# Optimization experiments

Measured on AMD Instinct MI355X. Metric: run time of the kernel, lower is better.

## Reference

```python
import jax, jax.numpy as jnp
import numpy as np

D_MODEL = 1024
D_STATE = 16
D_CONV = 4
EXPAND = 1
D_INNER = EXPAND * D_MODEL  # must equal D_MODEL for original dt_proj shapes to work
BATCH = 2
SEQ = 2048


def silu(x):
    return x * jax.nn.sigmoid(x)


def setup_inputs() -> dict:
    key = jax.random.key(0)
    ks = jax.random.split(key, 8)
    s = 0.02
    return {
        "x": jax.random.normal(ks[0], (BATCH, SEQ, D_MODEL), dtype=jnp.float32),
        "W_in": jax.random.normal(ks[1], (2 * D_INNER, D_MODEL), dtype=jnp.float32) * s,
        "conv_w": jax.random.normal(ks[2], (D_INNER, D_CONV), dtype=jnp.float32) * s,
        "conv_b": jnp.zeros((D_INNER,), dtype=jnp.float32),
        "W_dt": jax.random.normal(ks[3], (D_INNER, D_INNER), dtype=jnp.float32) * s,
        "b_dt": jnp.zeros((D_INNER,), dtype=jnp.float32),
        "A_log": jnp.zeros((D_INNER, D_STATE), dtype=jnp.float32),  # torch: log(ones)=0
        "Bp": jax.random.normal(ks[4], (D_INNER, D_STATE), dtype=jnp.float32),
        "Cp": jax.random.normal(ks[5], (D_INNER, D_STATE), dtype=jnp.float32),
        "Dp": jnp.ones((D_INNER,), dtype=jnp.float32),
        "W_out": jax.random.normal(ks[6], (D_MODEL, D_INNER), dtype=jnp.float32) * s,
    }


def reference(x, W_in, conv_w, conv_b, W_dt, b_dt, A_log, Bp, Cp, Dp, W_out):
    B, L, _ = x.shape
    # in_proj then split into ssm branch and gating residual
    xr = x @ W_in.T                               # (B, L, 2*D_INNER)
    x_proj, res = jnp.split(xr, 2, axis=-1)       # each (B, L, D_INNER)

    # causal depthwise conv1d (kernel D_CONV), == torch conv1d(padding=K-1)[..., :L]
    xp = jnp.pad(x_proj, ((0, 0), (D_CONV - 1, 0), (0, 0)))
    xc = conv_b + sum(conv_w[:, k] * xp[:, k:k + L, :] for k in range(D_CONV))
    xc = silu(xc)                                 # (B, L, D_INNER)

    # selective SSM scan
    delta = jax.nn.softplus(xc @ W_dt.T + b_dt)   # (B, L, D_INNER)
    A = -jnp.exp(A_log)                           # (D_INNER, D_STATE)
    dA = jnp.exp(delta[..., None] * A)            # (B, L, D_INNER, D_STATE)
    dBx = delta[..., None] * Bp * xc[..., None]   # (B, L, D_INNER, D_STATE)

    def step(h, inp):
        dA_t, dBx_t = inp                         # (B, D_INNER, D_STATE)
        h = dA_t * h + dBx_t
        y = jnp.einsum('bdn,dn->bd', h, Cp)
        return h, y

    h0 = jnp.zeros((B, D_INNER, D_STATE), dtype=x.dtype)
    _, ys = jax.lax.scan(step, h0, (dA.transpose(1, 0, 2, 3), dBx.transpose(1, 0, 2, 3)))
    x_ssm = ys.transpose(1, 0, 2) + xc * Dp       # (B, L, D_INNER)

    return (x_ssm * silu(res)) @ W_out.T          # (B, L, D_MODEL)
```

## Files before the change

### kernel.cpp

```cpp
#include <hip/hip_runtime.h>

typedef unsigned short u16;
typedef __bf16 bf16;
typedef bf16 bf16x8 __attribute__((ext_vector_type(8)));
typedef float f32x4 __attribute__((ext_vector_type(4)));

#define SEQ     2048
#define BATCH   2
#define DM      1024
#define DI      1024
#define NROW    (BATCH*SEQ)
#define NSTATE  16
#define NCHUNK  64
#define CLEN    32
#define BK      64

static_assert(SEQ == NCHUNK * CLEN, "chunking must cover SEQ");

__device__ __forceinline__ u16 f2bf(float f) {
  unsigned u = __builtin_bit_cast(unsigned, f);
  u += 0x7FFFu + ((u >> 16) & 1u);
  return (u16)(u >> 16);
}
__device__ __forceinline__ float bf2f(u16 u) {
  return __builtin_bit_cast(float, (unsigned)u << 16);
}
__device__ __forceinline__ float sigm(float x) { return 1.f / (1.f + __expf(-x)); }

__global__ __launch_bounds__(256) void k_cvt_all(
    const float* __restrict__ x, const float* __restrict__ Win,
    const float* __restrict__ Wdt, const float* __restrict__ Wout,
    u16* __restrict__ xbf, u16* __restrict__ winbf,
    u16* __restrict__ wdtbf, u16* __restrict__ woutbf)
{
  long i = (long)blockIdx.x * 256 + threadIdx.x;
  const float* src; u16* dst; long off;
  if (i < 1048576)            { src = x;    dst = xbf;    off = i; }
  else if (i < 1572864)       { src = Win;  dst = winbf;  off = i - 1048576; }
  else if (i < 1835008)       { src = Wdt;  dst = wdtbf;  off = i - 1572864; }
  else                        { src = Wout; dst = woutbf; off = i - 1835008; }
  float4 v = reinterpret_cast<const float4*>(src)[off];
  ushort4 o;
  o.x = f2bf(v.x); o.y = f2bf(v.y); o.z = f2bf(v.z); o.w = f2bf(v.w);
  reinterpret_cast<ushort4*>(dst)[off] = o;
}


__device__ __forceinline__ void gload16(const u16* g, u16* l) {
  __builtin_amdgcn_global_load_lds((const __attribute__((address_space(1))) void*)g,
                                   (__attribute__((address_space(3))) void*)l,
                                   16, 0, 0);
}

template<int EPI, int BM, int BN, int GX>
__global__ __launch_bounds__(256, 4) void k_gemm(
    const u16* __restrict__ A, const u16* __restrict__ B,
    float* __restrict__ outf, u16* __restrict__ outb,
    const float* __restrict__ bias, int M, int N, int K)
{
  constexpr int MI_ = BM / 32;
  constexpr int NI_ = BN / 32;
  __shared__ __align__(16) u16 sA[2 * BM * BK];
  __shared__ __align__(16) u16 sB[2 * BN * BK];
  const int t = threadIdx.x;
  const int wave = t >> 6, lane = t & 63;
  const int lr = lane & 15, kb = lane >> 4;
  const int wr = wave >> 1, wc = wave & 1;

  const int nwg = gridDim.x;
  const int bid = blockIdx.x;
  const int wg  = (bid & 7) * (nwg >> 3) + (bid >> 3);
  const long bm = (long)(wg / GX) * BM;
  const long bn = (long)(wg % GX) * BN;

  f32x4 acc[MI_][NI_] = {};

  const int srow = t >> 3;
  const int gslot8 = (((t & 7) ^ (srow & 7)) * 8);
  const u16* gA0 = A + (bm + srow) * (long)K + gslot8;
  const u16* gB0 = B + (bn + srow) * (long)K + gslot8;

  auto STAGE = [&](int buf, int k0) {
    #pragma unroll
    for (int i = 0; i < BM / 32; ++i)
      gload16(gA0 + (long)i * 32 * K + k0,
              &sA[buf * (BM * BK) + i * 2048 + wave * 512]);
    #pragma unroll
    for (int i = 0; i < BN / 32; ++i)
      gload16(gB0 + (long)i * 32 * K + k0,
              &sB[buf * (BN * BK) + i * 2048 + wave * 512]);
  };

  const int xr8 = (lr & 7) * 8;
  STAGE(0, 0);
  __syncthreads();
  int cur = 0;
  for (int k0 = 0; k0 < K; k0 += BK) {
    if (k0 + BK < K) STAGE(cur ^ 1, k0 + BK);
    const u16* pa = &sA[cur * (BM * BK)];
    const u16* pb = &sB[cur * (BN * BK)];
    bf16x8 af[2][MI_], bfr[2][NI_];
    #pragma unroll
    for (int kk = 0; kk < 2; ++kk) {
      const int co = ((kb * 8 + kk * 32) ^ xr8);
      #pragma unroll
      for (int mi = 0; mi < MI_; ++mi)
        af[kk][mi] = *reinterpret_cast<const bf16x8*>(
            pa + (wr * (BM / 2) + mi * 16 + lr) * BK + co);
      #pragma unroll
      for (int ni = 0; ni < NI_; ++ni)
        bfr[kk][ni] = *reinterpret_cast<const bf16x8*>(
            pb + (wc * (BN / 2) + ni * 16 + lr) * BK + co);
    }
    #pragma unroll
    for (int kk = 0; kk < 2; ++kk)
      #pragma unroll
      for (int mi = 0; mi < MI_; ++mi)
        #pragma unroll
        for (int ni = 0; ni < NI_; ++ni)
          acc[mi][ni] = __builtin_amdgcn_mfma_f32_16x16x32_bf16(
              af[kk][mi], bfr[kk][ni], acc[mi][ni], 0, 0, 0);
    __syncthreads();
    cur ^= 1;
  }

  #pragma unroll
  for (int mi = 0; mi < MI_; ++mi) {
    const long row0 = bm + wr * (BM / 2) + mi * 16 + kb * 4;
    #pragma unroll
    for (int ni = 0; ni < NI_; ++ni) {
      const long col = bn + wc * (BN / 2) + ni * 16 + lr;
      #pragma unroll
      for (int j = 0; j < 4; ++j) {
        const float v = acc[mi][ni][j];
        const long r = row0 + j;
        if (EPI == 0) {
          outf[r * N + col] = v;
        } else if (EPI == 1) {
          if (col < DI) outf[r * DI + col] = v;
          else          outb[r * DI + (col - DI)] = f2bf(v * sigm(v));
        } else {
          float z = v + bias[col];
          outb[r * N + col] = f2bf(fmaxf(z, 0.f) + log1pf(__expf(-fabsf(z))));
        }
      }
    }
  }
}

__global__ void k_conv(const float* __restrict__ xproj, const float* __restrict__ convw,
                       const float* __restrict__ convb, u16* __restrict__ xcbf)
{
  const int idx = blockIdx.x * 256 + threadIdx.x;
  const int d = idx & (DI - 1);
  const int m = idx >> 10;
  const int l = m & (SEQ - 1);
  float acc = convb[d];
  #pragma unroll
  for (int k = 0; k < 4; ++k) {
    int ls = l + k - 3;
    if (ls >= 0)
      acc = fmaf(convw[d * 4 + k], xproj[(long)(m + k - 3) * DI + d], acc);
  }
  float s = acc * sigm(acc);
  xcbf[idx] = f2bf(s);
}

__global__ __launch_bounds__(256) void k_scanA(
    const u16* __restrict__ delta, const u16* __restrict__ xc,
    const float* __restrict__ A_log, const float* __restrict__ Bp,
    float* __restrict__ hfin, float* __restrict__ sumdt_buf)
{
  const int tid = threadIdx.x, blk = blockIdx.x;
  const int d = (blk & 3) * 256 + tid;
  const int c = (blk >> 2) & (NCHUNK - 1);
  const int b = blk >> 8;
  float Aa[NSTATE], Bb[NSTATE], h[NSTATE];
  #pragma unroll
  for (int n = 0; n < NSTATE; ++n) {
    Aa[n] = -__expf(A_log[d * NSTATE + n]);
    Bb[n] = Bp[d * NSTATE + n];
    h[n] = 0.f;
  }
  const long base = ((long)(b * SEQ + c * CLEN)) * DI + d;
  float sdt = 0.f;
  for (int i = 0; i < CLEN; ++i) {
    float dt = bf2f(delta[base + (long)i * DI]);
    float x  = bf2f(xc[base + (long)i * DI]);
    sdt += dt;
    float dx = dt * x;
    #pragma unroll
    for (int n = 0; n < NSTATE; ++n) {
      float da = __expf(dt * Aa[n]);
      h[n] = fmaf(da, h[n], dx * Bb[n]);
    }
  }
  const long sb = ((long)(b * NCHUNK + c) * NSTATE) * DI + d;
  #pragma unroll
  for (int n = 0; n < NSTATE; ++n) hfin[sb + (long)n * DI] = h[n];
  sumdt_buf[(long)(b * NCHUNK + c) * DI + d] = sdt;
}

__global__ __launch_bounds__(256) void k_combine(
    const float* __restrict__ hfin, const float* __restrict__ sumdt_buf,
    const float* __restrict__ A_log, float* __restrict__ hstart)
{
  const int idx = blockIdx.x * 256 + threadIdx.x;
  const int d = idx & (DI - 1);
  const int n = (idx >> 10) & (NSTATE - 1);
  const int b = idx >> 14;
  const float Aa = -__expf(A_log[d * NSTATE + n]);
  float h = 0.f;
  for (int c = 0; c < NCHUNK; ++c) {
    const long sb = ((long)(b * NCHUNK + c) * NSTATE + n) * DI + d;
    hstart[sb] = h;
    float sdt = sumdt_buf[(long)(b * NCHUNK + c) * DI + d];
    h = fmaf(__expf(Aa * sdt), h, hfin[sb]);
  }
}

__global__ __launch_bounds__(256) void k_scanB(
    const u16* __restrict__ delta, const u16* __restrict__ xc,
    const float* __restrict__ A_log, const float* __restrict__ Bp,
    const float* __restrict__ Cp, const float* __restrict__ Dp,
    const u16* __restrict__ sres, const float* __restrict__ hstart,
    u16* __restrict__ gated)
{
  const int tid = threadIdx.x, blk = blockIdx.x;
  const int d = (blk & 3) * 256 + tid;
  const int c = (blk >> 2) & (NCHUNK - 1);
  const int b = blk >> 8;
  float Aa[NSTATE], Bb[NSTATE], Cc[NSTATE], h[NSTATE];
  #pragma unroll
  for (int n = 0; n < NSTATE; ++n) {
    Aa[n] = -__expf(A_log[d * NSTATE + n]);
    Bb[n] = Bp[d * NSTATE + n];
    Cc[n] = Cp[d * NSTATE + n];
  }
  const float Dd = Dp[d];
  const long sb = ((long)(b * NCHUNK + c) * NSTATE) * DI + d;
  #pragma unroll
  for (int n = 0; n < NSTATE; ++n) h[n] = hstart[sb + (long)n * DI];
  const long base = ((long)(b * SEQ + c * CLEN)) * DI + d;
  for (int i = 0; i < CLEN; ++i) {
    float dt = bf2f(delta[base + (long)i * DI]);
    float x  = bf2f(xc[base + (long)i * DI]);
    float dx = dt * x;
    float y = 0.f;
    #pragma unroll
    for (int n = 0; n < NSTATE; ++n) {
      float da = __expf(dt * Aa[n]);
      h[n] = fmaf(da, h[n], dx * Bb[n]);
      y = fmaf(h[n], Cc[n], y);
    }
    float xs = fmaf(x, Dd, y);
    float g = xs * bf2f(sres[base + (long)i * DI]);
    gated[base + (long)i * DI] = f2bf(g);
  }
}

extern "C" void kernel_launch(void* const* d_in, const int* in_sizes, int n_in,
                              void* d_out, int out_size, void* d_ws, size_t ws_size,
                              hipStream_t stream)
{
  const float* x      = (const float*)d_in[0];
  const float* W_in   = (const float*)d_in[1];
  const float* conv_w = (const float*)d_in[2];
  const float* conv_b = (const float*)d_in[3];
  const float* W_dt   = (const float*)d_in[4];
  const float* b_dt   = (const float*)d_in[5];
  const float* A_log  = (const float*)d_in[6];
  const float* Bp     = (const float*)d_in[7];
  const float* Cp     = (const float*)d_in[8];
  const float* Dp     = (const float*)d_in[9];
  const float* W_out  = (const float*)d_in[10];
  float* out = (float*)d_out;

  const long MD = (long)NROW * DI;

  char* ws = (char*)d_ws;
  float* x_proj   = (float*)ws;             ws += MD * 4;
  u16*   silu_bf  = (u16*)ws;               ws += MD * 2;
  u16*   delta_bf = (u16*)ws;               ws += MD * 2;
  u16*   xc_bf    = (u16*)ws;               ws += MD * 2;
  u16*   xbf      = (u16*)ws;               ws += MD * 2;
  u16*   Win_bf   = (u16*)ws;               ws += (long)2 * DI * DM * 2;
  u16*   Wdt_bf   = (u16*)ws;               ws += (long)DI * DI * 2;
  u16*   Wout_bf  = (u16*)ws;               ws += (long)DM * DI * 2;
  float* hfin     = (float*)ws;             ws += (long)BATCH * NCHUNK * NSTATE * DI * 4;
  float* sumdt    = (float*)ws;             ws += (long)BATCH * NCHUNK * DI * 4;
  float* hstart   = (float*)ws;             ws += (long)BATCH * NCHUNK * NSTATE * DI * 4;

  u16* gated = xbf;

  k_cvt_all<<<dim3(8192), dim3(256), 0, stream>>>(
      x, W_in, W_dt, W_out, xbf, Win_bf, Wdt_bf, Wout_bf);

  k_gemm<1, 128, 64, 32><<<dim3(1024), dim3(256), 0, stream>>>(
      xbf, Win_bf, x_proj, silu_bf, nullptr, NROW, 2 * DI, DM);

  k_conv<<<dim3((unsigned)(MD / 256)), dim3(256), 0, stream>>>(
      x_proj, conv_w, conv_b, xc_bf);

  k_gemm<2, 64, 64, 16><<<dim3(1024), dim3(256), 0, stream>>>(
      xc_bf, Wdt_bf, nullptr, delta_bf, b_dt, NROW, DI, DI);

  k_scanA<<<dim3(BATCH * NCHUNK * (DI / 256)), dim3(256), 0, stream>>>(
      delta_bf, xc_bf, A_log, Bp, hfin, sumdt);
  k_combine<<<dim3(BATCH * NSTATE * DI / 256), dim3(256), 0, stream>>>(
      hfin, sumdt, A_log, hstart);
  k_scanB<<<dim3(BATCH * NCHUNK * (DI / 256)), dim3(256), 0, stream>>>(
      delta_bf, xc_bf, A_log, Bp, Cp, Dp, silu_bf, hstart, gated);

  k_gemm<0, 64, 64, 16><<<dim3(1024), dim3(256), 0, stream>>>(
      gated, Wout_bf, out, nullptr, nullptr, NROW, DM, DI);
}
```

Baseline: 161.9 us.

## Switch GEMMs to 32x32x16 MFMA, enlarge in_proj tile, store x_proj as bf16

Rewrites the GEMM inner loop to use 32x32x16 bf16 MFMA with 16-wide accumulators, and splits the epilogue to match the new lane layout. The in_proj GEMM uses 128x128 tiles with fewer blocks, and launch bounds are lowered to 2 to allow more registers. The x_proj half of the in_proj output is now written as bf16 and read as bf16 by the conv kernel, halving that traffic at some cost in precision.

```diff
diff --git a/kernel.cpp b/kernel.cpp
--- a/kernel.cpp
+++ b/kernel.cpp
@@ -3,7 +3,7 @@
 typedef unsigned short u16;
 typedef __bf16 bf16;
 typedef bf16 bf16x8 __attribute__((ext_vector_type(8)));
-typedef float f32x4 __attribute__((ext_vector_type(4)));
+typedef float f32x16 __attribute__((ext_vector_type(16)));
 
 #define SEQ     2048
 #define BATCH   2
@@ -53,18 +53,18 @@
 }
 
 template<int EPI, int BM, int BN, int GX>
-__global__ __launch_bounds__(256, 4) void k_gemm(
+__global__ __launch_bounds__(256, 2) void k_gemm(
     const u16* __restrict__ A, const u16* __restrict__ B,
-    float* __restrict__ outf, u16* __restrict__ outb,
+    float* __restrict__ outf, u16* __restrict__ outb, u16* __restrict__ outb2,
     const float* __restrict__ bias, int M, int N, int K)
 {
-  constexpr int MI_ = BM / 32;
-  constexpr int NI_ = BN / 32;
+  constexpr int MI_ = BM / 64;
+  constexpr int NI_ = BN / 64;
   __shared__ __align__(16) u16 sA[2 * BM * BK];
   __shared__ __align__(16) u16 sB[2 * BN * BK];
   const int t = threadIdx.x;
   const int wave = t >> 6, lane = t & 63;
-  const int lr = lane & 15, kb = lane >> 4;
+  const int la = lane & 31, hi = lane >> 5;
   const int wr = wave >> 1, wc = wave & 1;
 
   const int nwg = gridDim.x;
@@ -73,7 +73,7 @@
   const long bm = (long)(wg / GX) * BM;
   const long bn = (long)(wg % GX) * BN;
 
-  f32x4 acc[MI_][NI_] = {};
+  f32x16 acc[MI_][NI_] = {};
 
   const int srow = t >> 3;
   const int gslot8 = (((t & 7) ^ (srow & 7)) * 8);
@@ -91,7 +91,7 @@
               &sB[buf * (BN * BK) + i * 2048 + wave * 512]);
   };
 
-  const int xr8 = (lr & 7) * 8;
+  const int xr = la & 7;
   STAGE(0, 0);
   __syncthreads();
   int cur = 0;
@@ -99,56 +99,58 @@
     if (k0 + BK < K) STAGE(cur ^ 1, k0 + BK);
     const u16* pa = &sA[cur * (BM * BK)];
     const u16* pb = &sB[cur * (BN * BK)];
-    bf16x8 af[2][MI_], bfr[2][NI_];
-    #pragma unroll
-    for (int kk = 0; kk < 2; ++kk) {
-      const int co = ((kb * 8 + kk * 32) ^ xr8);
+    bf16x8 af[4][MI_], bfr[4][NI_];
+    #pragma unroll
+    for (int ks = 0; ks < 4; ++ks) {
+      const int co = ((ks * 2 + hi) ^ xr) * 8;
       #pragma unroll
       for (int mi = 0; mi < MI_; ++mi)
-        af[kk][mi] = *reinterpret_cast<const bf16x8*>(
-            pa + (wr * (BM / 2) + mi * 16 + lr) * BK + co);
+        af[ks][mi] = *reinterpret_cast<const bf16x8*>(
+            pa + (wr * (BM / 2) + mi * 32 + la) * BK + co);
       #pragma unroll
       for (int ni = 0; ni < NI_; ++ni)
-        bfr[kk][ni] = *reinterpret_cast<const bf16x8*>(
-            pb + (wc * (BN / 2) + ni * 16 + lr) * BK + co);
+        bfr[ks][ni] = *reinterpret_cast<const bf16x8*>(
+            pb + (wc * (BN / 2) + ni * 32 + la) * BK + co);
     }
     #pragma unroll
-    for (int kk = 0; kk < 2; ++kk)
+    for (int ks = 0; ks < 4; ++ks)
       #pragma unroll
       for (int mi = 0; mi < MI_; ++mi)
         #pragma unroll
         for (int ni = 0; ni < NI_; ++ni)
-          acc[mi][ni] = __builtin_amdgcn_mfma_f32_16x16x32_bf16(
-              af[kk][mi], bfr[kk][ni], acc[mi][ni], 0, 0, 0);
+          acc[mi][ni] = __builtin_amdgcn_mfma_f32_32x32x16_bf16(
+              af[ks][mi], bfr[ks][ni], acc[mi][ni], 0, 0, 0);
     __syncthreads();
     cur ^= 1;
   }
 
   #pragma unroll
   for (int mi = 0; mi < MI_; ++mi) {
-    const long row0 = bm + wr * (BM / 2) + mi * 16 + kb * 4;
+    const long rowb = bm + wr * (BM / 2) + mi * 32 + 4 * hi;
     #pragma unroll
     for (int ni = 0; ni < NI_; ++ni) {
-      const long col = bn + wc * (BN / 2) + ni * 16 + lr;
+      const long col = bn + wc * (BN / 2) + ni * 32 + la;
       #pragma unroll
-      for (int j = 0; j < 4; ++j) {
-        const float v = acc[mi][ni][j];
-        const long r = row0 + j;
-        if (EPI == 0) {
-          outf[r * N + col] = v;
-        } else if (EPI == 1) {
-          if (col < DI) outf[r * DI + col] = v;
-          else          outb[r * DI + (col - DI)] = f2bf(v * sigm(v));
-        } else {
-          float z = v + bias[col];
-          outb[r * N + col] = f2bf(fmaxf(z, 0.f) + log1pf(__expf(-fabsf(z))));
+      for (int q = 0; q < 4; ++q)
+        #pragma unroll
+        for (int j = 0; j < 4; ++j) {
+          const float v = acc[mi][ni][q * 4 + j];
+          const long r = rowb + q * 8 + j;
+          if (EPI == 0) {
+            outf[r * N + col] = v;
+          } else if (EPI == 1) {
+            if (bn < DI) outb[r * DI + col] = f2bf(v);
+            else         outb2[r * DI + (col - DI)] = f2bf(v * sigm(v));
+          } else {
+            float z = v + bias[col];
+            outb[r * N + col] = f2bf(fmaxf(z, 0.f) + log1pf(__expf(-fabsf(z))));
+          }
         }
-      }
     }
   }
 }
 
-__global__ void k_conv(const float* __restrict__ xproj, const float* __restrict__ convw,
+__global__ void k_conv(const u16* __restrict__ xproj, const float* __restrict__ convw,
                        const float* __restrict__ convb, u16* __restrict__ xcbf)
 {
   const int idx = blockIdx.x * 256 + threadIdx.x;
@@ -160,7 +162,7 @@
   for (int k = 0; k < 4; ++k) {
     int ls = l + k - 3;
     if (ls >= 0)
-      acc = fmaf(convw[d * 4 + k], xproj[(long)(m + k - 3) * DI + d], acc);
+      acc = fmaf(convw[d * 4 + k], bf2f(xproj[(long)(m + k - 3) * DI + d]), acc);
   }
   float s = acc * sigm(acc);
   xcbf[idx] = f2bf(s);
@@ -279,7 +281,7 @@
   const long MD = (long)NROW * DI;
 
   char* ws = (char*)d_ws;
-  float* x_proj   = (float*)ws;             ws += MD * 4;
+  u16*   xproj_bf = (u16*)ws;               ws += MD * 2;
   u16*   silu_bf  = (u16*)ws;               ws += MD * 2;
   u16*   delta_bf = (u16*)ws;               ws += MD * 2;
   u16*   xc_bf    = (u16*)ws;               ws += MD * 2;
@@ -296,14 +298,14 @@
   k_cvt_all<<<dim3(8192), dim3(256), 0, stream>>>(
       x, W_in, W_dt, W_out, xbf, Win_bf, Wdt_bf, Wout_bf);
 
-  k_gemm<1, 128, 64, 32><<<dim3(1024), dim3(256), 0, stream>>>(
-      xbf, Win_bf, x_proj, silu_bf, nullptr, NROW, 2 * DI, DM);
+  k_gemm<1, 128, 128, 16><<<dim3(512), dim3(256), 0, stream>>>(
+      xbf, Win_bf, nullptr, xproj_bf, silu_bf, nullptr, NROW, 2 * DI, DM);
 
   k_conv<<<dim3((unsigned)(MD / 256)), dim3(256), 0, stream>>>(
-      x_proj, conv_w, conv_b, xc_bf);
+      xproj_bf, conv_w, conv_b, xc_bf);
 
   k_gemm<2, 64, 64, 16><<<dim3(1024), dim3(256), 0, stream>>>(
-      xc_bf, Wdt_bf, nullptr, delta_bf, b_dt, NROW, DI, DI);
+      xc_bf, Wdt_bf, nullptr, delta_bf, nullptr, b_dt, NROW, DI, DI);
 
   k_scanA<<<dim3(BATCH * NCHUNK * (DI / 256)), dim3(256), 0, stream>>>(
       delta_bf, xc_bf, A_log, Bp, hfin, sumdt);
@@ -313,5 +315,5 @@
       delta_bf, xc_bf, A_log, Bp, Cp, Dp, silu_bf, hstart, gated);
 
   k_gemm<0, 64, 64, 16><<<dim3(1024), dim3(256), 0, stream>>>(
-      gated, Wout_bf, out, nullptr, nullptr, NROW, DM, DI);
-}
+      gated, Wout_bf, out, nullptr, nullptr, nullptr, NROW, DM, DI);
+}
```

New measurement: 157.2 us. 2.9% less time.
